# Kernel tuning notes

Hardware: AMD Instinct MI355X
Metric: run time of the kernel (lower is better)

Reference implementation:

```python
import jax, jax.numpy as jnp
import numpy as np

EPS = 1e-5  # torch BatchNorm2d default eps
K = 3       # kernel_size
D = 1       # dilation (== padding)


def setup_inputs() -> dict:
    key = jax.random.key(0)
    k0, k1, k2 = jax.random.split(key, 3)
    N, C, H, W, O = 4, 2048, 32, 32, 256
    return {
        "x": jax.random.normal(k0, (N, C, H, W), jnp.float32),
        "conv_w": jax.random.normal(k1, (K * K, C, K, K), jnp.float32) * 0.01,
        "gamma": jnp.ones((K * K,), jnp.float32),
        "beta": jnp.zeros((K * K,), jnp.float32),
        "weight": jax.random.normal(k2, (O, C, K * K), jnp.float32) * 0.01,
    }


def reference(x, conv_w, gamma, beta, weight):
    n, c, h, w = x.shape
    # --- dynamic-kernel generator: conv (stride 1, pad=dilation) -> BN (train mode) -> softmax over K*K ---
    sigma = jax.lax.conv_general_dilated(
        x, conv_w, window_strides=(1, 1), padding=[(D, D), (D, D)],
        rhs_dilation=(D, D), dimension_numbers=("NCHW", "OIHW", "NCHW"))  # (n, K*K, h, w)
    mean = sigma.mean(axis=(0, 2, 3), keepdims=True)
    var = sigma.var(axis=(0, 2, 3), keepdims=True)  # biased variance, as torch BN uses for normalization
    sigma = (sigma - mean) * jax.lax.rsqrt(var + EPS)
    sigma = sigma * gamma[None, :, None, None] + beta[None, :, None, None]
    sigma = jax.nn.softmax(sigma, axis=1)            # softmax over the K*K kernel positions
    sigma = sigma.reshape(n, K * K, h * w)           # (n, K*K, h*w)
    # --- unfold (im2col), channel-major (C, kh, kw) ordering matching torch F.unfold ---
    patches = jax.lax.conv_general_dilated_patches(
        x, (K, K), (1, 1), [(D, D), (D, D)], rhs_dilation=(D, D),
        dimension_numbers=("NCHW", "OIHW", "NCHW"))  # (n, C*K*K, h, w)
    patches = patches.reshape(n, c, K * K, h * w)     # (n, C, K*K, h*w)
    # --- per-pixel dynamic weighting + learned projection ---
    # out[n,o,m] = sum_{c,l} patches[n,c,l,m] * sigma[n,l,m] * weight[o,c,l]
    out = jnp.einsum("nclm,nlm,ocl->nom", patches, sigma, weight)
    return out.reshape(n, weight.shape[0], h, w)
```

## Files before the change

### kernel.cpp

```cpp
#include <hip/hip_runtime.h>
#include <hip/hip_bf16.h>
#include <stdint.h>

typedef unsigned short u16;
typedef __attribute__((ext_vector_type(8))) short short8;
typedef __attribute__((ext_vector_type(4))) float floatx4;

#define N_IMG 4
#define C_IN  2048
#define HW    1024
#define KK    9
#define O_OUT 256
#define NPIX  4096
#define M_PAD  2560
#define H_ROWS 2432
#define K_DIM  2048
#define BN_EPS 1e-5f

#define OFF_A    0u
#define OFF_XT   10485760u
#define OFF_H    27262976u
#define OFF_SRAW 47185920u
#define OFF_STAT 47333376u

__device__ __forceinline__ u16 f2b(float f) {
    unsigned u = __float_as_uint(f);
    return (u16)((u + 0x7FFFu + ((u >> 16) & 1u)) >> 16);
}

__device__ __forceinline__ void load8f(const float* base, size_t eidx, u16* out) {
    const float* p = base + eidx;
    float4 a = ((const float4*)p)[0];
    float4 b = ((const float4*)p)[1];
    float f[8] = {a.x, a.y, a.z, a.w, b.x, b.y, b.z, b.w};
#pragma unroll
    for (int j = 0; j < 8; ++j) out[j] = f2b(f[j]);
}

__global__ void build_all(const float* __restrict__ x, const float* __restrict__ wgt,
                          const float* __restrict__ cw, u16* __restrict__ xt,
                          u16* __restrict__ A, float* __restrict__ stats) {
    __shared__ __align__(16) u16 lds[9 * 2056];
    int b = blockIdx.x, t = threadIdx.x;
    if (b < 2048) {
        int c0 = (b & 31) * 64, p0 = ((b >> 5) & 15) * 64, n = b >> 9;
        int rp = t >> 3;
        int pv = (t & 7) * 8;
        u16 h0[8], h1[8];
        load8f(x, (size_t)(n * C_IN + c0 + 2 * rp) * HW + p0 + pv, h0);
        load8f(x, (size_t)(n * C_IN + c0 + 2 * rp + 1) * HW + p0 + pv, h1);
        unsigned* l32 = (unsigned*)lds;
#pragma unroll
        for (int j = 0; j < 8; ++j)
            l32[(pv + j) * 35 + rp] = (unsigned)h0[j] | ((unsigned)h1[j] << 16);
        __syncthreads();
        int pr = t >> 3, cq = (t & 7) * 4;
        unsigned o0[4], o1[4];
#pragma unroll
        for (int i = 0; i < 4; ++i) {
            o0[i] = l32[pr * 35 + cq + i];
            o1[i] = l32[(pr + 32) * 35 + cq + i];
        }
        *(uint4*)(xt + (size_t)(n * HW + p0 + pr) * K_DIM + c0 + cq * 2) = *(uint4*)o0;
        *(uint4*)(xt + (size_t)(n * HW + p0 + pr + 32) * K_DIM + c0 + cq * 2) = *(uint4*)o1;
    } else if (b < 2304) {
        int o = b - 2048;
        size_t base = (size_t)o * 18432;
        for (int i = 0; i < 9; ++i) {
            int e0 = (t + i * 256) * 8;
            u16 hv[8];
            load8f(wgt, base + e0, hv);
#pragma unroll
            for (int j = 0; j < 8; ++j) {
                int e = e0 + j;
                int c = e / 9, l = e - c * 9;
                lds[l * 2056 + c] = hv[j];
            }
        }
        __syncthreads();
        for (int l = 0; l < 9; ++l) {
            size_t row = (size_t)l * 256 + o;
            *(uint4*)(A + row * K_DIM + t * 8) = *(const uint4*)&lds[l * 2056 + t * 8];
        }
    } else if (b < 2313) {
        int l = b - 2304;
        size_t base = (size_t)l * 18432;
        for (int i = 0; i < 9; ++i) {
            int e0 = (t + i * 256) * 8;
            u16 hv[8];
            load8f(cw, base + e0, hv);
#pragma unroll
            for (int j = 0; j < 8; ++j) {
                int e = e0 + j;
                int c = e / 9, k = e - c * 9;
                lds[k * 2056 + c] = hv[j];
            }
        }
        __syncthreads();
        for (int k = 0; k < 9; ++k) {
            size_t row = 2304 + (size_t)k * 9 + l;
            *(uint4*)(A + row * K_DIM + t * 8) = *(const uint4*)&lds[k * 2056 + t * 8];
        }
    } else {
        uint4 z = {0, 0, 0, 0};
        uint4* dst = (uint4*)(A + (size_t)2385 * K_DIM);
        for (int i = t; i < (47 * 2048) / 8; i += 256) dst[i] = z;
        if (t < 18) stats[t] = 0.0f;
    }
}

__device__ __forceinline__ void gload_lds16(const void* g, void* l) {
    __builtin_amdgcn_global_load_lds((__attribute__((address_space(1))) void*)(g),
                                     (__attribute__((address_space(3))) void*)(l), 16, 0, 0);
}

#define STG(gbase, ldsarr, bb, hh, kt) do {                                                        \
    gload_lds16((gbase) + (size_t)((hh) * 128 + (w * 2 + 0) * 8) * K_DIM + (size_t)(kt) * 64,      \
                (ldsarr) + (bb) * 16384 + (hh) * 8192 + ldsw);                                     \
    gload_lds16((gbase) + (size_t)((hh) * 128 + (w * 2 + 1) * 8) * K_DIM + (size_t)(kt) * 64,      \
                (ldsarr) + (bb) * 16384 + (hh) * 8192 + ldsw + 512);                               \
} while (0)

#define RD_A(bb, mi, ks) (*(const short8*)(As + (bb) * 16384 + arow + (mi) * 1024 + col[ks]))
#define RD_B(bb, ni, ks) (*(const short8*)(Bs + (bb) * 16384 + brow + (ni) * 1024 + col[ks]))

#define READ_BALL(bb) do {                                                   \
    bq[0][0] = RD_B(bb, 0, 0); bq[0][1] = RD_B(bb, 0, 1);                    \
    bq[1][0] = RD_B(bb, 1, 0); bq[1][1] = RD_B(bb, 1, 1);                    \
    bq[2][0] = RD_B(bb, 2, 0); bq[2][1] = RD_B(bb, 2, 1);                    \
    bq[3][0] = RD_B(bb, 3, 0); bq[3][1] = RD_B(bb, 3, 1);                    \
} while (0)

#define READ_AQ(bb, qd) do {                                                 \
    aq[0][0] = RD_A(bb, 2 * (qd), 0);     aq[0][1] = RD_A(bb, 2 * (qd), 1);  \
    aq[1][0] = RD_A(bb, 2 * (qd) + 1, 0); aq[1][1] = RD_A(bb, 2 * (qd) + 1, 1); \
} while (0)

#define MFMA1(mi, ni, ks) acc[mi][ni] = __builtin_amdgcn_mfma_f32_16x16x32_bf16( \
    aq[(mi) & 1][ks], bq[ni][ks], acc[mi][ni], 0, 0, 0)

#define MFMA_Q(qd) do {                                                                      \
    MFMA1(2*(qd),   0, 0); MFMA1(2*(qd),   1, 0); MFMA1(2*(qd),   2, 0); MFMA1(2*(qd),   3, 0); \
    MFMA1(2*(qd)+1, 0, 0); MFMA1(2*(qd)+1, 1, 0); MFMA1(2*(qd)+1, 2, 0); MFMA1(2*(qd)+1, 3, 0); \
    MFMA1(2*(qd),   0, 1); MFMA1(2*(qd),   1, 1); MFMA1(2*(qd),   2, 1); MFMA1(2*(qd),   3, 1); \
    MFMA1(2*(qd)+1, 0, 1); MFMA1(2*(qd)+1, 1, 1); MFMA1(2*(qd)+1, 2, 1); MFMA1(2*(qd)+1, 3, 1); \
} while (0)

#define BAR1_MFMA(qd) do {                                   \
    __builtin_amdgcn_s_barrier();                            \
    asm volatile("s_waitcnt lgkmcnt(0)" ::: "memory");       \
    __builtin_amdgcn_sched_barrier(0);                       \
    __builtin_amdgcn_s_setprio(1);                           \
    MFMA_Q(qd);                                              \
    __builtin_amdgcn_s_setprio(0);                           \
} while (0)
#define BAR2() __builtin_amdgcn_s_barrier()
#define VMW4() asm volatile("s_waitcnt vmcnt(4)" ::: "memory")
#define VMW0() asm volatile("s_waitcnt vmcnt(0)" ::: "memory")

__global__ __launch_bounds__(512, 2) void gemm_bt(const u16* __restrict__ A,
                                                  const u16* __restrict__ B,
                                                  __hip_bfloat16* __restrict__ C) {
    __shared__ __align__(16) u16 As[2 * 256 * 64];
    __shared__ __align__(16) u16 Bs[2 * 256 * 64];

    int orig = blockIdx.x;
    int wgid = (orig & 7) * 20 + (orig >> 3);
    int mt = wgid % 10, nt = wgid / 10;
    int m0 = mt * 256, n0 = nt * 256;

    int t = threadIdx.x;
    int w = t >> 6, L = t & 63;
    int wm = w >> 2, wn = w & 3;
    int q = L >> 4, lm = L & 15;
    int lr = L >> 3, ls = L & 7;

    int csw = (ls ^ lr) * 8;
    const u16* gA0 = A + (size_t)(m0 + lr) * K_DIM + csw;
    const u16* gB0 = B + (size_t)(n0 + lr) * K_DIM + csw;
    int ldsw = w * 1024;

    int sw = (lm & 7) << 3;
    int arow = (wm * 128 + lm) * 64;
    int brow = (wn * 64 + lm) * 64;
    int col[2] = { (q * 8) ^ sw, (32 + q * 8) ^ sw };

    floatx4 acc[8][4];
    floatx4 z = {0.f, 0.f, 0.f, 0.f};
#pragma unroll
    for (int i = 0; i < 8; ++i)
#pragma unroll
        for (int j = 0; j < 4; ++j) acc[i][j] = z;

    short8 aq[2][2], bq[4][2];

    STG(gA0, As, 0, 0, 0); STG(gA0, As, 0, 1, 0);
    STG(gB0, Bs, 0, 0, 0); STG(gB0, Bs, 0, 1, 0);
    STG(gB0, Bs, 1, 0, 1); STG(gB0, Bs, 1, 1, 1);
    VMW4();
    BAR2();

    for (int it = 0; it < 15; ++it) {
        int T = 2 * it;
        READ_BALL(0); READ_AQ(0, 0);
        STG(gA0, As, 1, 0, T + 1); STG(gA0, As, 1, 1, T + 1);
        BAR1_MFMA(0); BAR2();
        READ_AQ(0, 1);
        STG(gB0, Bs, 0, 0, T + 2);
        BAR1_MFMA(1); BAR2();
        READ_AQ(0, 2);
        STG(gB0, Bs, 0, 1, T + 2);
        BAR1_MFMA(2); BAR2();
        READ_AQ(0, 3);
        BAR1_MFMA(3); VMW4(); BAR2();
        READ_BALL(1); READ_AQ(1, 0);
        STG(gA0, As, 0, 0, T + 2); STG(gA0, As, 0, 1, T + 2);
        BAR1_MFMA(0); BAR2();
        READ_AQ(1, 1);
        STG(gB0, Bs, 1, 0, T + 3);
        BAR1_MFMA(1); BAR2();
        READ_AQ(1, 2);
        STG(gB0, Bs, 1, 1, T + 3);
        BAR1_MFMA(2); BAR2();
        READ_AQ(1, 3);
        BAR1_MFMA(3); VMW4(); BAR2();
    }

    READ_BALL(0); READ_AQ(0, 0);
    STG(gA0, As, 1, 0, 31); STG(gA0, As, 1, 1, 31);
    BAR1_MFMA(0); BAR2();
    READ_AQ(0, 1); BAR1_MFMA(1); BAR2();
    READ_AQ(0, 2); BAR1_MFMA(2); BAR2();
    READ_AQ(0, 3); BAR1_MFMA(3); VMW0(); BAR2();
    READ_BALL(1); READ_AQ(1, 0); BAR1_MFMA(0); BAR2();
    READ_AQ(1, 1); BAR1_MFMA(1); BAR2();
    READ_AQ(1, 2); BAR1_MFMA(2); BAR2();
    READ_AQ(1, 3); BAR1_MFMA(3); BAR2();

    if (m0 + 255 < H_ROWS) {
#pragma unroll
        for (int mi = 0; mi < 8; ++mi) {
            int gm = m0 + wm * 128 + mi * 16 + q * 4;
#pragma unroll
            for (int ni = 0; ni < 4; ++ni) {
                int gn = n0 + wn * 64 + ni * 16 + lm;
#pragma unroll
                for (int r = 0; r < 4; ++r)
                    C[(size_t)(gm + r) * NPIX + gn] = __float2bfloat16(acc[mi][ni][r]);
            }
        }
    } else {
#pragma unroll
        for (int mi = 0; mi < 8; ++mi) {
            int gm = m0 + wm * 128 + mi * 16 + q * 4;
#pragma unroll
            for (int ni = 0; ni < 4; ++ni) {
                int gn = n0 + wn * 64 + ni * 16 + lm;
#pragma unroll
                for (int r = 0; r < 4; ++r) {
                    int row = gm + r;
                    if (row < H_ROWS)
                        C[(size_t)row * NPIX + gn] = __float2bfloat16(acc[mi][ni][r]);
                }
            }
        }
    }
}

__global__ void sigma_stats(const __hip_bfloat16* __restrict__ Hm, float* __restrict__ sraw,
                            float* __restrict__ stats) {
    int b = blockIdx.x;
    int qq = b & 3, nl = b >> 2;
    int n = nl / 9, l = nl - n * 9;
    int t = threadIdx.x;
    int pix = qq * 256 + t;
    int y = pix >> 5, x = pix & 31;
    float v = 0.f;
#pragma unroll
    for (int k = 0; k < 9; ++k) {
        int yy = y + k / 3 - 1, xx = x + (k % 3) - 1;
        if (yy >= 0 && yy < 32 && xx >= 0 && xx < 32)
            v += __bfloat162float(Hm[(size_t)(2304 + k * 9 + l) * NPIX + n * HW + yy * 32 + xx]);
    }
    sraw[(size_t)nl * HW + pix] = v;
    __shared__ float r1[256], r2[256];
    r1[t] = v; r2[t] = v * v;
    __syncthreads();
    for (int s = 128; s > 0; s >>= 1) {
        if (t < s) { r1[t] += r1[t + s]; r2[t] += r2[t + s]; }
        __syncthreads();
    }
    if (t == 0) { atomicAdd(&stats[l], r1[0]); atomicAdd(&stats[9 + l], r2[0]); }
}

__global__ void tail(const __hip_bfloat16* __restrict__ Hm, const float* __restrict__ sraw,
                     const float* __restrict__ stats, const float* __restrict__ gamma,
                     const float* __restrict__ beta, float* __restrict__ out) {
    int b = blockIdx.x;
    int n = b >> 8, rem = b & 255;
    int ph = rem >> 7, og = rem & 127;
    int t = threadIdx.x;
    float mean[9], istd[9], gg[9], bb[9];
#pragma unroll
    for (int l = 0; l < 9; ++l) {
        float m = stats[l] * (1.f / 4096.f);
        float var = stats[9 + l] * (1.f / 4096.f) - m * m;
        mean[l] = m; istd[l] = rsqrtf(var + BN_EPS);
        gg[l] = gamma[l]; bb[l] = beta[l];
    }
    const __hip_bfloat16* hb = Hm + (size_t)(og * 2) * NPIX + (size_t)n * HW;
    float* ob = out + ((size_t)n * 256 + og * 2) * HW;
#pragma unroll
    for (int i = 0; i < 2; ++i) {
        int pix = ph * 512 + i * 256 + t;
        int y = pix >> 5, x = pix & 31;
        float v[9];
        float mx = -1e30f;
#pragma unroll
        for (int l = 0; l < 9; ++l) {
            float tv = (sraw[(size_t)(n * 9 + l) * HW + pix] - mean[l]) * istd[l];
            tv = tv * gg[l] + bb[l];
            v[l] = tv; mx = fmaxf(mx, tv);
        }
        float ssum = 0.f;
#pragma unroll
        for (int l = 0; l < 9; ++l) { v[l] = __expf(v[l] - mx); ssum += v[l]; }
        float inv = 1.f / ssum;
        float acc0 = 0.f, acc1 = 0.f;
#pragma unroll
        for (int l = 0; l < 9; ++l) {
            int dy = l / 3 - 1, dx = l % 3 - 1;
            int yy = y + dy, xx = x + dx;
            if (yy >= 0 && yy < 32 && xx >= 0 && xx < 32) {
                float sv = v[l] * inv;
                size_t hidx = (size_t)(l * 256) * NPIX + (size_t)(pix + dy * 32 + dx);
                acc0 += sv * __bfloat162float(hb[hidx]);
                acc1 += sv * __bfloat162float(hb[hidx + NPIX]);
            }
        }
        ob[pix] = acc0;
        ob[HW + pix] = acc1;
    }
}

extern "C" void kernel_launch(void* const* d_in, const int* in_sizes, int n_in,
                              void* d_out, int out_size, void* d_ws, size_t ws_size,
                              hipStream_t stream) {
    const float* x     = (const float*)d_in[0];
    const float* cw    = (const float*)d_in[1];
    const float* gamma = (const float*)d_in[2];
    const float* beta  = (const float*)d_in[3];
    const float* wgt   = (const float*)d_in[4];

    char* ws = (char*)d_ws;
    u16*   Abuf = (u16*)(ws + OFF_A);
    u16*   XT   = (u16*)(ws + OFF_XT);
    u16*   Hm   = (u16*)(ws + OFF_H);
    float* sraw = (float*)(ws + OFF_SRAW);
    float* stats= (float*)(ws + OFF_STAT);

    build_all<<<2314, 256, 0, stream>>>(x, wgt, cw, XT, Abuf, stats);
    gemm_bt<<<160, 512, 0, stream>>>(Abuf, XT, (__hip_bfloat16*)Hm);
    sigma_stats<<<N_IMG * KK * 4, 256, 0, stream>>>((const __hip_bfloat16*)Hm, sraw, stats);
    tail<<<1024, 256, 0, stream>>>((const __hip_bfloat16*)Hm, sraw, stats, gamma, beta, (float*)d_out);
}
```

Before: 173.8 us.

## Drop redundant GEMM barriers and lgkmcnt waits, reorder LDS reads and MFMAs

Removes the second barrier after most MFMA quarter-blocks and drops the explicit lgkmcnt(0) wait and sched_barrier. Barriers are replaced with compiler memory fences around s_barrier, so the compiler inserts the waits it needs. LDS reads and MFMAs are reordered so the first k-slice operands arrive first and MFMAs alternate between the two A rows. This aims to cut synchronisation stalls and let MFMAs start earlier, but removing barriers risks WAR races between the async global-to-LDS stages and the reads of the same buffer still in flight in other waves.

New measurement: 170.9 us. Within noise of the previous version (-1.7%).

```diff
diff --git a/kernel.cpp b/kernel.cpp
--- a/kernel.cpp
+++ b/kernel.cpp
@@ -125,36 +125,36 @@
 #define RD_B(bb, ni, ks) (*(const short8*)(Bs + (bb) * 16384 + brow + (ni) * 1024 + col[ks]))
 
 #define READ_BALL(bb) do {                                                   \
-    bq[0][0] = RD_B(bb, 0, 0); bq[0][1] = RD_B(bb, 0, 1);                    \
-    bq[1][0] = RD_B(bb, 1, 0); bq[1][1] = RD_B(bb, 1, 1);                    \
-    bq[2][0] = RD_B(bb, 2, 0); bq[2][1] = RD_B(bb, 2, 1);                    \
-    bq[3][0] = RD_B(bb, 3, 0); bq[3][1] = RD_B(bb, 3, 1);                    \
+    bq[0][0] = RD_B(bb, 0, 0); bq[1][0] = RD_B(bb, 1, 0);                    \
+    bq[2][0] = RD_B(bb, 2, 0); bq[3][0] = RD_B(bb, 3, 0);                    \
+    bq[0][1] = RD_B(bb, 0, 1); bq[1][1] = RD_B(bb, 1, 1);                    \
+    bq[2][1] = RD_B(bb, 2, 1); bq[3][1] = RD_B(bb, 3, 1);                    \
 } while (0)
 
 #define READ_AQ(bb, qd) do {                                                 \
-    aq[0][0] = RD_A(bb, 2 * (qd), 0);     aq[0][1] = RD_A(bb, 2 * (qd), 1);  \
-    aq[1][0] = RD_A(bb, 2 * (qd) + 1, 0); aq[1][1] = RD_A(bb, 2 * (qd) + 1, 1); \
+    aq[0][0] = RD_A(bb, 2 * (qd), 0);     aq[1][0] = RD_A(bb, 2 * (qd) + 1, 0); \
+    aq[0][1] = RD_A(bb, 2 * (qd), 1);     aq[1][1] = RD_A(bb, 2 * (qd) + 1, 1); \
 } while (0)
 
 #define MFMA1(mi, ni, ks) acc[mi][ni] = __builtin_amdgcn_mfma_f32_16x16x32_bf16( \
     aq[(mi) & 1][ks], bq[ni][ks], acc[mi][ni], 0, 0, 0)
 
 #define MFMA_Q(qd) do {                                                                      \
-    MFMA1(2*(qd),   0, 0); MFMA1(2*(qd),   1, 0); MFMA1(2*(qd),   2, 0); MFMA1(2*(qd),   3, 0); \
-    MFMA1(2*(qd)+1, 0, 0); MFMA1(2*(qd)+1, 1, 0); MFMA1(2*(qd)+1, 2, 0); MFMA1(2*(qd)+1, 3, 0); \
-    MFMA1(2*(qd),   0, 1); MFMA1(2*(qd),   1, 1); MFMA1(2*(qd),   2, 1); MFMA1(2*(qd),   3, 1); \
-    MFMA1(2*(qd)+1, 0, 1); MFMA1(2*(qd)+1, 1, 1); MFMA1(2*(qd)+1, 2, 1); MFMA1(2*(qd)+1, 3, 1); \
-} while (0)
+    MFMA1(2*(qd),   0, 0); MFMA1(2*(qd)+1, 0, 0); MFMA1(2*(qd),   1, 0); MFMA1(2*(qd)+1, 1, 0); \
+    MFMA1(2*(qd),   2, 0); MFMA1(2*(qd)+1, 2, 0); MFMA1(2*(qd),   3, 0); MFMA1(2*(qd)+1, 3, 0); \
+    MFMA1(2*(qd),   0, 1); MFMA1(2*(qd)+1, 0, 1); MFMA1(2*(qd),   1, 1); MFMA1(2*(qd)+1, 1, 1); \
+    MFMA1(2*(qd),   2, 1); MFMA1(2*(qd)+1, 2, 1); MFMA1(2*(qd),   3, 1); MFMA1(2*(qd)+1, 3, 1); \
+} while (0)
+
+#define FENCE() asm volatile("" ::: "memory")
+#define BARRIER() do { FENCE(); __builtin_amdgcn_s_barrier(); FENCE(); } while (0)
 
 #define BAR1_MFMA(qd) do {                                   \
-    __builtin_amdgcn_s_barrier();                            \
-    asm volatile("s_waitcnt lgkmcnt(0)" ::: "memory");       \
-    __builtin_amdgcn_sched_barrier(0);                       \
+    BARRIER();                                               \
     __builtin_amdgcn_s_setprio(1);                           \
     MFMA_Q(qd);                                              \
     __builtin_amdgcn_s_setprio(0);                           \
 } while (0)
-#define BAR2() __builtin_amdgcn_s_barrier()
 #define VMW4() asm volatile("s_waitcnt vmcnt(4)" ::: "memory")
 #define VMW0() asm volatile("s_waitcnt vmcnt(0)" ::: "memory")
 
@@ -198,44 +198,46 @@
     STG(gB0, Bs, 0, 0, 0); STG(gB0, Bs, 0, 1, 0);
     STG(gB0, Bs, 1, 0, 1); STG(gB0, Bs, 1, 1, 1);
     VMW4();
-    BAR2();
+    BARRIER();
 
     for (int it = 0; it < 15; ++it) {
         int T = 2 * it;
-        READ_BALL(0); READ_AQ(0, 0);
+        READ_AQ(0, 0); READ_BALL(0);
         STG(gA0, As, 1, 0, T + 1); STG(gA0, As, 1, 1, T + 1);
-        BAR1_MFMA(0); BAR2();
+        BAR1_MFMA(0);
+        BARRIER();
         READ_AQ(0, 1);
         STG(gB0, Bs, 0, 0, T + 2);
-        BAR1_MFMA(1); BAR2();
+        BAR1_MFMA(1);
         READ_AQ(0, 2);
         STG(gB0, Bs, 0, 1, T + 2);
-        BAR1_MFMA(2); BAR2();
+        BAR1_MFMA(2);
         READ_AQ(0, 3);
-        BAR1_MFMA(3); VMW4(); BAR2();
-        READ_BALL(1); READ_AQ(1, 0);
+        BAR1_MFMA(3); VMW4(); BARRIER();
+        READ_AQ(1, 0); READ_BALL(1);
         STG(gA0, As, 0, 0, T + 2); STG(gA0, As, 0, 1, T + 2);
-        BAR1_MFMA(0); BAR2();
+        BAR1_MFMA(0);
+        BARRIER();
         READ_AQ(1, 1);
         STG(gB0, Bs, 1, 0, T + 3);
-        BAR1_MFMA(1); BAR2();
+        BAR1_MFMA(1);
         READ_AQ(1, 2);
         STG(gB0, Bs, 1, 1, T + 3);
-        BAR1_MFMA(2); BAR2();
+        BAR1_MFMA(2);
         READ_AQ(1, 3);
-        BAR1_MFMA(3); VMW4(); BAR2();
-    }
-
-    READ_BALL(0); READ_AQ(0, 0);
+        BAR1_MFMA(3); VMW4(); BARRIER();
+    }
+
+    READ_AQ(0, 0); READ_BALL(0);
     STG(gA0, As, 1, 0, 31); STG(gA0, As, 1, 1, 31);
-    BAR1_MFMA(0); BAR2();
-    READ_AQ(0, 1); BAR1_MFMA(1); BAR2();
-    READ_AQ(0, 2); BAR1_MFMA(2); BAR2();
-    READ_AQ(0, 3); BAR1_MFMA(3); VMW0(); BAR2();
-    READ_BALL(1); READ_AQ(1, 0); BAR1_MFMA(0); BAR2();
-    READ_AQ(1, 1); BAR1_MFMA(1); BAR2();
-    READ_AQ(1, 2); BAR1_MFMA(2); BAR2();
-    READ_AQ(1, 3); BAR1_MFMA(3); BAR2();
+    BAR1_MFMA(0);
+    READ_AQ(0, 1); BAR1_MFMA(1);
+    READ_AQ(0, 2); BAR1_MFMA(2);
+    READ_AQ(0, 3); BAR1_MFMA(3); VMW0(); BARRIER();
+    READ_AQ(1, 0); READ_BALL(1); BAR1_MFMA(0);
+    READ_AQ(1, 1); BAR1_MFMA(1);
+    READ_AQ(1, 2); BAR1_MFMA(2);
+    READ_AQ(1, 3); BAR1_MFMA(3);
 
     if (m0 + 255 < H_ROWS) {
 #pragma unroll
```
